# Kernel optimization log

Measured on AMD Instinct MI355X. Metric: run time of the kernel, lower is better.

## Reference

```python
import jax, jax.numpy as jnp
import numpy as np


def setup_inputs() -> dict:
    key = jax.random.key(0)
    ks = jax.random.split(key, 5)
    B, T, D = 1, 4096, 1024
    scale = 0.02
    return {
        "x": jax.random.normal(ks[0], (B, T, D), dtype=jnp.float32),
        "Wq": jax.random.normal(ks[1], (D, D), dtype=jnp.float32) * scale,
        "Wk": jax.random.normal(ks[2], (D, D), dtype=jnp.float32) * scale,
        "Wv": jax.random.normal(ks[3], (D, D), dtype=jnp.float32) * scale,
        "Wo": jax.random.normal(ks[4], (D, D), dtype=jnp.float32) * scale,
        "window": 128,
    }


def reference(x, Wq, Wk, Wv, Wo, window):
    # x: [B, T, D]; weights: [D, D] (torch nn.Linear layout: out = x @ W.T)
    B, T, D = x.shape
    H = 16
    dh = D // H

    def split_heads(y):
        # [B, T, D] -> [B, H, T, dh]
        return y.reshape(B, T, H, dh).transpose(0, 2, 1, 3)

    q = split_heads(x @ Wq.T)
    k = split_heads(x @ Wk.T)
    v = split_heads(x @ Wv.T)

    # causal sliding-window additive mask, [T, T]
    idx = jnp.arange(T)
    diff = idx[:, None] - idx[None, :]
    allowed = (diff >= 0) & (diff <= window)

    scale = 1.0 / jnp.sqrt(jnp.asarray(dh, dtype=q.dtype))
    scores = jnp.einsum('bhtd,bhsd->bhts', q, k) * scale  # [B,H,T,T]
    scores = jnp.where(allowed[None, None], scores, jnp.asarray(-jnp.inf, dtype=scores.dtype))
    attn = jax.nn.softmax(scores, axis=-1)
    out = jnp.einsum('bhts,bhsd->bhtd', attn, v)  # [B,H,T,dh]
    out = out.transpose(0, 2, 1, 3).reshape(B, T, D)
    return out @ Wo.T
```

## Files before the change

kernel.cpp:

```cpp
#include <hip/hip_runtime.h>
#include <hip/hip_bf16.h>

typedef __bf16 bf16_t;
typedef __bf16 bf16x8 __attribute__((ext_vector_type(8)));
typedef float f32x4 __attribute__((ext_vector_type(4)));

#define T_SEQ 4096
#define DM    1024
#define NH    16
#define DH    64

#define BM 128
#define BN 128
#define BK 64

typedef __attribute__((address_space(1))) void gvoid_t;
typedef __attribute__((address_space(3))) void lvoid_t;

__device__ __forceinline__ void gload_lds16(const void* g, void* l) {
    __builtin_amdgcn_global_load_lds((gvoid_t*)g, (lvoid_t*)l, 16, 0, 0);
}

__global__ __launch_bounds__(256) void cvt_all(
    const float* __restrict__ x,  const float* __restrict__ wq,
    const float* __restrict__ wk, const float* __restrict__ wv,
    const float* __restrict__ wo,
    bf16_t* __restrict__ xb, bf16_t* __restrict__ wqb, bf16_t* __restrict__ wkb,
    bf16_t* __restrict__ wvb, bf16_t* __restrict__ wob)
{
    const float* s; bf16_t* d; int n8;
    switch (blockIdx.y) {
        case 0:  s = x;  d = xb;  n8 = (T_SEQ * DM) / 8; break;
        case 1:  s = wq; d = wqb; n8 = (DM * DM) / 8;    break;
        case 2:  s = wk; d = wkb; n8 = (DM * DM) / 8;    break;
        case 3:  s = wv; d = wvb; n8 = (DM * DM) / 8;    break;
        default: s = wo; d = wob; n8 = (DM * DM) / 8;    break;
    }
    for (int i = blockIdx.x * 256 + threadIdx.x; i < n8; i += gridDim.x * 256) {
        float4 a = ((const float4*)s)[i * 2];
        float4 b = ((const float4*)s)[i * 2 + 1];
        bf16x8 o;
        o[0] = (bf16_t)a.x; o[1] = (bf16_t)a.y; o[2] = (bf16_t)a.z; o[3] = (bf16_t)a.w;
        o[4] = (bf16_t)b.x; o[5] = (bf16_t)b.y; o[6] = (bf16_t)b.z; o[7] = (bf16_t)b.w;
        ((bf16x8*)d)[i] = o;
    }
}

__global__ __launch_bounds__(256) void gemm_bt(
    const bf16_t* __restrict__ A,
    const bf16_t* __restrict__ B0, const bf16_t* __restrict__ B1, const bf16_t* __restrict__ B2,
    bf16_t* __restrict__ C0, bf16_t* __restrict__ C1, bf16_t* __restrict__ C2,
    int M, int N, int K)
{
    const bf16_t* Bp; bf16_t* Cp;
    if      (blockIdx.z == 0) { Bp = B0; Cp = C0; }
    else if (blockIdx.z == 1) { Bp = B1; Cp = C1; }
    else                      { Bp = B2; Cp = C2; }

    __shared__ __align__(16) bf16_t sA[BM * BK];
    __shared__ __align__(16) bf16_t sB[BN * BK];

    const int tid  = threadIdx.x;
    const int lane = tid & 63;
    const int w    = tid >> 6;
    const int wr   = w >> 1, wc = w & 1;
    const int l15  = lane & 15, lhi = lane >> 4;

    const int brow = blockIdx.x * BM;
    const int bcol = blockIdx.y * BN;

    f32x4 acc[4][4] = {};

    const int nkt = K / BK;
    for (int kt = 0; kt < nkt; ++kt) {
        __syncthreads();
        #pragma unroll
        for (int i = 0; i < 4; ++i) {
            int chunk = i * 256 + tid;
            int row   = chunk >> 3;
            int c8    = chunk & 7;
            int c8s   = c8 ^ (row & 7);
            const bf16_t* gA = A  + (size_t)(brow + row) * K + kt * BK + c8s * 8;
            const bf16_t* gB = Bp + (size_t)(bcol + row) * K + kt * BK + c8s * 8;
            gload_lds16(gA, &sA[chunk * 8]);
            gload_lds16(gB, &sB[chunk * 8]);
        }
        __syncthreads();

        #pragma unroll
        for (int kk = 0; kk < 2; ++kk) {
            bf16x8 af[4], bfr[4];
            #pragma unroll
            for (int m = 0; m < 4; ++m) {
                int r  = wr * 64 + m * 16 + l15;
                int c8 = (kk * 4 + lhi) ^ (r & 7);
                af[m] = *(const bf16x8*)(&sA[r * BK + c8 * 8]);
            }
            #pragma unroll
            for (int n = 0; n < 4; ++n) {
                int r  = wc * 64 + n * 16 + l15;
                int c8 = (kk * 4 + lhi) ^ (r & 7);
                bfr[n] = *(const bf16x8*)(&sB[r * BK + c8 * 8]);
            }
            #pragma unroll
            for (int m = 0; m < 4; ++m)
                #pragma unroll
                for (int n = 0; n < 4; ++n)
                    acc[m][n] = __builtin_amdgcn_mfma_f32_16x16x32_bf16(
                        af[m], bfr[n], acc[m][n], 0, 0, 0);
        }
    }

    #pragma unroll
    for (int m = 0; m < 4; ++m) {
        int rb = brow + wr * 64 + m * 16 + lhi * 4;
        #pragma unroll
        for (int n = 0; n < 4; ++n) {
            int cc = bcol + wc * 64 + n * 16 + l15;
            #pragma unroll
            for (int i = 0; i < 4; ++i)
                Cp[(size_t)(rb + i) * N + cc] = (bf16_t)acc[m][n][i];
        }
    }
}

__global__ __launch_bounds__(256) void gemm_bt_64(
    const bf16_t* __restrict__ A, const bf16_t* __restrict__ B,
    float* __restrict__ C, int M, int N, int K)
{
    __shared__ __align__(16) bf16_t sA[64 * BK];
    __shared__ __align__(16) bf16_t sB[128 * BK];

    const int tid  = threadIdx.x;
    const int lane = tid & 63;
    const int w    = tid >> 6;
    const int wr   = w >> 1, wc = w & 1;
    const int l15  = lane & 15, lhi = lane >> 4;

    const int brow = blockIdx.x * 64;
    const int bcol = blockIdx.y * 128;

    f32x4 acc[2][4] = {};

    const int nkt = K / BK;
    for (int kt = 0; kt < nkt; ++kt) {
        __syncthreads();
        #pragma unroll
        for (int i = 0; i < 6; ++i) {
            int chunk = i * 256 + tid;
            if (chunk < 512) {
                int row = chunk >> 3, c8 = chunk & 7;
                int c8s = c8 ^ (row & 7);
                gload_lds16(A + (size_t)(brow + row) * K + kt * BK + c8s * 8,
                            &sA[chunk * 8]);
            } else {
                int bc  = chunk - 512;
                int row = bc >> 3, c8 = bc & 7;
                int c8s = c8 ^ (row & 7);
                gload_lds16(B + (size_t)(bcol + row) * K + kt * BK + c8s * 8,
                            &sB[bc * 8]);
            }
        }
        __syncthreads();

        #pragma unroll
        for (int kk = 0; kk < 2; ++kk) {
            bf16x8 af[2], bfr[4];
            #pragma unroll
            for (int m = 0; m < 2; ++m) {
                int r  = wr * 32 + m * 16 + l15;
                int c8 = (kk * 4 + lhi) ^ (r & 7);
                af[m] = *(const bf16x8*)(&sA[r * BK + c8 * 8]);
            }
            #pragma unroll
            for (int n = 0; n < 4; ++n) {
                int r  = wc * 64 + n * 16 + l15;
                int c8 = (kk * 4 + lhi) ^ (r & 7);
                bfr[n] = *(const bf16x8*)(&sB[r * BK + c8 * 8]);
            }
            #pragma unroll
            for (int m = 0; m < 2; ++m)
                #pragma unroll
                for (int n = 0; n < 4; ++n)
                    acc[m][n] = __builtin_amdgcn_mfma_f32_16x16x32_bf16(
                        af[m], bfr[n], acc[m][n], 0, 0, 0);
        }
    }

    #pragma unroll
    for (int m = 0; m < 2; ++m) {
        int rb = brow + wr * 32 + m * 16 + lhi * 4;
        #pragma unroll
        for (int n = 0; n < 4; ++n) {
            int cc = bcol + wc * 64 + n * 16 + l15;
            #pragma unroll
            for (int i = 0; i < 4; ++i)
                C[(size_t)(rb + i) * N + cc] = acc[m][n][i];
        }
    }
}

#define PPAD 72
__global__ __launch_bounds__(256) void swa_attn(
    const bf16_t* __restrict__ Q, const bf16_t* __restrict__ K,
    const bf16_t* __restrict__ V, bf16_t* __restrict__ O,
    const int* __restrict__ winp)
{
    const int w    = winp[0];
    const int tid  = threadIdx.x;
    const int lane = tid & 63;
    const int wv   = tid >> 6;
    const int l15  = lane & 15, lhi = lane >> 4;
    const int h    = blockIdx.y;
    const int q0   = blockIdx.x * 128 + wv * 32;

    __shared__ __align__(16) bf16_t Pl[4][32 * PPAD];
    bf16_t* Pw = &Pl[wv][0];

    const bf16_t* Qh = Q + (size_t)h * DH;
    const bf16_t* Kh = K + (size_t)h * DH;
    const bf16_t* Vh = V + (size_t)h * DH;

    bf16x8 qf[2][2];
    #pragma unroll
    for (int g = 0; g < 2; ++g)
        #pragma unroll
        for (int c = 0; c < 2; ++c)
            qf[g][c] = *(const bf16x8*)(Qh + (size_t)(q0 + g * 16 + l15) * DM
                                           + c * 32 + lhi * 8);

    f32x4 acc[2][4] = {};
    f32x4 mrow[2], lrow[2];
    #pragma unroll
    for (int g = 0; g < 2; ++g) {
        mrow[g] = { -1e30f, -1e30f, -1e30f, -1e30f };
        lrow[g] = {};
    }

    int ks = q0 - w; if (ks < 0) ks = 0; ks &= ~63;
    for (int kvs = ks; kvs <= q0 + 31; kvs += 64) {
        f32x4 s[2][4];
        #pragma unroll
        for (int hc = 0; hc < 4; ++hc) {
            bf16x8 kf[2];
            #pragma unroll
            for (int c = 0; c < 2; ++c)
                kf[c] = *(const bf16x8*)(Kh + (size_t)(kvs + hc * 16 + l15) * DM
                                            + c * 32 + lhi * 8);
            #pragma unroll
            for (int g = 0; g < 2; ++g) {
                f32x4 z = {};
                z = __builtin_amdgcn_mfma_f32_16x16x32_bf16(qf[g][0], kf[0], z, 0, 0, 0);
                z = __builtin_amdgcn_mfma_f32_16x16x32_bf16(qf[g][1], kf[1], z, 0, 0, 0);
                #pragma unroll
                for (int i = 0; i < 4; ++i) {
                    int qt = q0 + g * 16 + lhi * 4 + i;
                    int kt = kvs + hc * 16 + l15;
                    bool ok = (kt <= qt) && (qt - kt <= w);
                    s[g][hc][i] = ok ? z[i] * 0.125f : -1e30f;
                }
            }
        }
        #pragma unroll
        for (int g = 0; g < 2; ++g) {
            f32x4 pm;
            #pragma unroll
            for (int i = 0; i < 4; ++i)
                pm[i] = fmaxf(fmaxf(s[g][0][i], s[g][1][i]),
                              fmaxf(s[g][2][i], s[g][3][i]));
            #pragma unroll
            for (int off = 1; off <= 8; off <<= 1)
                #pragma unroll
                for (int i = 0; i < 4; ++i)
                    pm[i] = fmaxf(pm[i], __shfl_xor(pm[i], off));

            f32x4 mnew, alpha, rs;
            #pragma unroll
            for (int i = 0; i < 4; ++i) {
                mnew[i]  = fmaxf(mrow[g][i], pm[i]);
                alpha[i] = __expf(mrow[g][i] - mnew[i]);
                rs[i]    = 0.f;
            }
            #pragma unroll
            for (int hc = 0; hc < 4; ++hc)
                #pragma unroll
                for (int i = 0; i < 4; ++i) {
                    float p = __expf(s[g][hc][i] - mnew[i]);
                    s[g][hc][i] = p;
                    rs[i] += p;
                }
            #pragma unroll
            for (int off = 1; off <= 8; off <<= 1)
                #pragma unroll
                for (int i = 0; i < 4; ++i)
                    rs[i] += __shfl_xor(rs[i], off);
            #pragma unroll
            for (int i = 0; i < 4; ++i) {
                lrow[g][i] = lrow[g][i] * alpha[i] + rs[i];
                mrow[g][i] = mnew[i];
            }
            #pragma unroll
            for (int nc = 0; nc < 4; ++nc)
                #pragma unroll
                for (int i = 0; i < 4; ++i) acc[g][nc][i] *= alpha[i];

            #pragma unroll
            for (int hc = 0; hc < 4; ++hc)
                #pragma unroll
                for (int i = 0; i < 4; ++i)
                    Pw[(g * 16 + lhi * 4 + i) * PPAD + hc * 16 + l15] =
                        (bf16_t)s[g][hc][i];
        }

        bf16x8 pa[2][2];
        #pragma unroll
        for (int g = 0; g < 2; ++g)
            #pragma unroll
            for (int kk = 0; kk < 2; ++kk)
                pa[g][kk] = *(const bf16x8*)(&Pw[(g * 16 + l15) * PPAD
                                                + kk * 32 + lhi * 8]);
        #pragma unroll
        for (int kk = 0; kk < 2; ++kk)
            #pragma unroll
            for (int nc = 0; nc < 4; ++nc) {
                bf16x8 vf;
                #pragma unroll
                for (int j = 0; j < 8; ++j)
                    vf[j] = Vh[(size_t)(kvs + kk * 32 + lhi * 8 + j) * DM
                               + nc * 16 + l15];
                #pragma unroll
                for (int g = 0; g < 2; ++g)
                    acc[g][nc] = __builtin_amdgcn_mfma_f32_16x16x32_bf16(
                        pa[g][kk], vf, acc[g][nc], 0, 0, 0);
            }
    }

    #pragma unroll
    for (int g = 0; g < 2; ++g)
        #pragma unroll
        for (int nc = 0; nc < 4; ++nc)
            #pragma unroll
            for (int i = 0; i < 4; ++i) {
                float o = acc[g][nc][i] / lrow[g][i];
                O[(size_t)(q0 + g * 16 + lhi * 4 + i) * DM + h * DH
                  + nc * 16 + l15] = (bf16_t)o;
            }
}

extern "C" void kernel_launch(void* const* d_in, const int* in_sizes, int n_in,
                              void* d_out, int out_size, void* d_ws, size_t ws_size,
                              hipStream_t stream)
{
    const float* x  = (const float*)d_in[0];
    const float* Wq = (const float*)d_in[1];
    const float* Wk = (const float*)d_in[2];
    const float* Wv = (const float*)d_in[3];
    const float* Wo = (const float*)d_in[4];
    const int*   wn = (const int*)d_in[5];
    float* out = (float*)d_out;

    bf16_t* ws = (bf16_t*)d_ws;
    const size_t nx = (size_t)T_SEQ * DM;
    const size_t nw = (size_t)DM * DM;
    bf16_t* xb  = ws;
    bf16_t* Wqb = xb + nx;
    bf16_t* Wkb = Wqb + nw;
    bf16_t* Wvb = Wkb + nw;
    bf16_t* Wob = Wvb + nw;
    bf16_t* Qb  = Wob + nw;
    bf16_t* Kb  = Qb + nx;
    bf16_t* Vb  = Kb + nx;
    bf16_t* Ab  = Vb + nx;

    dim3 g0(512, 5, 1);
    cvt_all<<<g0, 256, 0, stream>>>(x, Wq, Wk, Wv, Wo, xb, Wqb, Wkb, Wvb, Wob);

    dim3 g1(T_SEQ / BM, DM / BN, 3);
    gemm_bt<<<g1, 256, 0, stream>>>(xb, Wqb, Wkb, Wvb, Qb, Kb, Vb, T_SEQ, DM, DM);

    dim3 g2(T_SEQ / 128, NH, 1);
    swa_attn<<<g2, 256, 0, stream>>>(Qb, Kb, Vb, Ab, wn);

    dim3 g3(T_SEQ / 64, DM / 128, 1);
    gemm_bt_64<<<g3, 256, 0, stream>>>(Ab, Wob, out, T_SEQ, DM, DM);
}
```

Baseline: 80.94 us.

## Compute V transposed via separate GEMM for contiguous PV operand loads

The V projection is split out of the fused QKV GEMM and computed as Wv·xᵀ, which stores V transposed (head-dim major, sequence contiguous). The attention kernel can then load each 8-element bf16 MFMA B operand with one vector load instead of eight strided scalar loads. The cost is an extra kernel launch and a GEMM with different tiling (64x128, writing bf16) in place of part of the fused launch.

```diff
diff --git a/kernel.cpp b/kernel.cpp
--- a/kernel.cpp
+++ b/kernel.cpp
@@ -48,14 +48,13 @@
 
 __global__ __launch_bounds__(256) void gemm_bt(
     const bf16_t* __restrict__ A,
-    const bf16_t* __restrict__ B0, const bf16_t* __restrict__ B1, const bf16_t* __restrict__ B2,
-    bf16_t* __restrict__ C0, bf16_t* __restrict__ C1, bf16_t* __restrict__ C2,
+    const bf16_t* __restrict__ B0, const bf16_t* __restrict__ B1,
+    bf16_t* __restrict__ C0, bf16_t* __restrict__ C1,
     int M, int N, int K)
 {
     const bf16_t* Bp; bf16_t* Cp;
-    if      (blockIdx.z == 0) { Bp = B0; Cp = C0; }
-    else if (blockIdx.z == 1) { Bp = B1; Cp = C1; }
-    else                      { Bp = B2; Cp = C2; }
+    if (blockIdx.z == 0) { Bp = B0; Cp = C0; }
+    else                 { Bp = B1; Cp = C1; }
 
     __shared__ __align__(16) bf16_t sA[BM * BK];
     __shared__ __align__(16) bf16_t sB[BN * BK];
@@ -124,9 +123,10 @@
     }
 }
 
+template<typename OT>
 __global__ __launch_bounds__(256) void gemm_bt_64(
     const bf16_t* __restrict__ A, const bf16_t* __restrict__ B,
-    float* __restrict__ C, int M, int N, int K)
+    OT* __restrict__ C, int M, int N, int K)
 {
     __shared__ __align__(16) bf16_t sA[64 * BK];
     __shared__ __align__(16) bf16_t sB[128 * BK];
@@ -195,7 +195,7 @@
             int cc = bcol + wc * 64 + n * 16 + l15;
             #pragma unroll
             for (int i = 0; i < 4; ++i)
-                C[(size_t)(rb + i) * N + cc] = acc[m][n][i];
+                C[(size_t)(rb + i) * N + cc] = (OT)acc[m][n][i];
         }
     }
 }
@@ -203,7 +203,7 @@
 #define PPAD 72
 __global__ __launch_bounds__(256) void swa_attn(
     const bf16_t* __restrict__ Q, const bf16_t* __restrict__ K,
-    const bf16_t* __restrict__ V, bf16_t* __restrict__ O,
+    const bf16_t* __restrict__ VT, bf16_t* __restrict__ O,
     const int* __restrict__ winp)
 {
     const int w    = winp[0];
@@ -217,9 +217,9 @@
     __shared__ __align__(16) bf16_t Pl[4][32 * PPAD];
     bf16_t* Pw = &Pl[wv][0];
 
-    const bf16_t* Qh = Q + (size_t)h * DH;
-    const bf16_t* Kh = K + (size_t)h * DH;
-    const bf16_t* Vh = V + (size_t)h * DH;
+    const bf16_t* Qh  = Q  + (size_t)h * DH;
+    const bf16_t* Kh  = K  + (size_t)h * DH;
+    const bf16_t* VTh = VT + (size_t)h * DH * T_SEQ;
 
     bf16x8 qf[2][2];
     #pragma unroll
@@ -323,11 +323,8 @@
         for (int kk = 0; kk < 2; ++kk)
             #pragma unroll
             for (int nc = 0; nc < 4; ++nc) {
-                bf16x8 vf;
-                #pragma unroll
-                for (int j = 0; j < 8; ++j)
-                    vf[j] = Vh[(size_t)(kvs + kk * 32 + lhi * 8 + j) * DM
-                               + nc * 16 + l15];
+                bf16x8 vf = *(const bf16x8*)(VTh + (size_t)(nc * 16 + l15) * T_SEQ
+                                                 + kvs + kk * 32 + lhi * 8);
                 #pragma unroll
                 for (int g = 0; g < 2; ++g)
                     acc[g][nc] = __builtin_amdgcn_mfma_f32_16x16x32_bf16(
@@ -369,18 +366,21 @@
     bf16_t* Wob = Wvb + nw;
     bf16_t* Qb  = Wob + nw;
     bf16_t* Kb  = Qb + nx;
-    bf16_t* Vb  = Kb + nx;
-    bf16_t* Ab  = Vb + nx;
+    bf16_t* VTb = Kb + nx;
+    bf16_t* Ab  = VTb + nx;
 
     dim3 g0(512, 5, 1);
     cvt_all<<<g0, 256, 0, stream>>>(x, Wq, Wk, Wv, Wo, xb, Wqb, Wkb, Wvb, Wob);
 
-    dim3 g1(T_SEQ / BM, DM / BN, 3);
-    gemm_bt<<<g1, 256, 0, stream>>>(xb, Wqb, Wkb, Wvb, Qb, Kb, Vb, T_SEQ, DM, DM);
+    dim3 g1(T_SEQ / BM, DM / BN, 2);
+    gemm_bt<<<g1, 256, 0, stream>>>(xb, Wqb, Wkb, Qb, Kb, T_SEQ, DM, DM);
+
+    dim3 gv(DM / 64, T_SEQ / 128, 1);
+    gemm_bt_64<bf16_t><<<gv, 256, 0, stream>>>(Wvb, xb, VTb, DM, T_SEQ, DM);
 
     dim3 g2(T_SEQ / 128, NH, 1);
-    swa_attn<<<g2, 256, 0, stream>>>(Qb, Kb, Vb, Ab, wn);
+    swa_attn<<<g2, 256, 0, stream>>>(Qb, Kb, VTb, Ab, wn);
 
     dim3 g3(T_SEQ / 64, DM / 128, 1);
-    gemm_bt_64<<<g3, 256, 0, stream>>>(Ab, Wob, out, T_SEQ, DM, DM);
-}
+    gemm_bt_64<float><<<g3, 256, 0, stream>>>(Ab, Wob, out, T_SEQ, DM, DM);
+}
```

New measurement: 93.28 us. 15.2% more time.
